# Optimization experiments

Hardware: AMD Instinct MI355X
Metric: run time of the kernel (lower is better)

## Reference

```python
import jax, jax.numpy as jnp
import numpy as np

LMAX = 10
F_IN = 64
F_OUT = 64
N_GRID = 512
IRREP_DIM = sum((2 * l + 1) ** 2 for l in range(LMAX + 1))  # 1771
BATCH = 256


def setup_inputs() -> dict:
    key = jax.random.key(0)
    kx, kD, kw = jax.random.split(key, 3)
    x = jax.random.normal(kx, (BATCH, F_IN, IRREP_DIM), dtype=jnp.float32)
    D = jax.random.normal(kD, (N_GRID, IRREP_DIM), dtype=jnp.float32)
    w = jax.random.normal(kw, (F_IN, F_OUT, N_GRID), dtype=jnp.float32)
    return {"x": x, "D": D, "w": w}


def _so3_linear(x, psi):
    # x:   (B, f_in, sum_l (2l+1)^2) signal over SO(3) irreps
    # psi: (f_in, f_out, sum_l (2l+1)^2) per-degree block weights
    B, f_in, _ = x.shape
    f_out = psi.shape[1]
    outs = []
    off = 0
    for l in range(LMAX + 1):
        d = 2 * l + 1
        blk = d * d
        # input block: multiplicity u (=d) x irrep component m (=d)
        x_l = x[:, :, off:off + blk].reshape(B, f_in, d, d)        # (B,i,u,m)
        w_l = psi[:, :, off:off + blk].reshape(f_in, f_out, d, d)  # (i,o,u,v)
        alpha = 1.0 / np.sqrt(f_in * d)  # e3nn fan-in path normalization
        out_l = jnp.einsum('bium,iouv->bovm', x_l, w_l) * alpha
        outs.append(out_l.reshape(B, f_out, blk))
        off += blk
    return jnp.concatenate(outs, axis=-1)


def reference(x, D, w):
    # project spatial filter into Fourier (irrep) domain
    n_grid = D.shape[0]
    psi = jnp.einsum('ni,xyn->xyi', D, w) / np.sqrt(n_grid)  # (f_in, f_out, IRREP_DIM)
    return _so3_linear(x, psi)
```

## Files before the change

kernel.cpp:

```cpp
#include <hip/hip_runtime.h>
#include <hip/hip_bf16.h>

#define IDIM 1771
#define NF 64
#define NG 512

constexpr int OFFS[12] = {0, 1, 10, 35, 84, 165, 286, 455, 680, 969, 1330, 1771};

typedef float f32x4 __attribute__((ext_vector_type(4)));
typedef float f32x2 __attribute__((ext_vector_type(2)));
typedef __bf16 bf16x2 __attribute__((ext_vector_type(2)));
typedef __bf16 bf16x8 __attribute__((ext_vector_type(8)));

__device__ __forceinline__ void gl_lds16(const void* g, void* l) {
    __builtin_amdgcn_global_load_lds((const __attribute__((address_space(1))) void*)g,
                                     (__attribute__((address_space(3))) void*)l, 16, 0, 0);
}

__global__ __launch_bounds__(256) void prep_repack_kernel(const float* __restrict__ D,
                                                          const float* __restrict__ w,
                                                          const float* __restrict__ x,
                                                          __bf16* __restrict__ Dt,
                                                          __bf16* __restrict__ wb,
                                                          __hip_bfloat16* __restrict__ A) {
    __shared__ alignas(16) char smem[16640];
    const int blk = blockIdx.x;
    const int t = threadIdx.x;
    const int lane = t & 63, grp = t >> 6;

    if (blk < 224) {
        float (*T)[65] = (float (*)[65])smem;
        const int ct = blk >> 3, nt = blk & 7;
        const int c0 = ct * 64, n0 = nt * 64;
        for (int nn = grp; nn < 64; nn += 4) {
            int c = c0 + lane;
            T[nn][lane] = (c < IDIM) ? D[(n0 + nn) * IDIM + c] : 0.0f;
        }
        __syncthreads();
        for (int cc = grp; cc < 64; cc += 4) {
            int c = c0 + cc;
            if (c < IDIM) Dt[c * NG + n0 + lane] = (__bf16)T[lane][cc];
        }
    } else if (blk < 288) {
        const int o = blk - 224;
#pragma unroll 4
        for (int ii = 0; ii < 64; ++ii) {
            f32x2 v = *(const f32x2*)&w[((size_t)(ii * 64 + o)) * NG + t * 2];
            bf16x2 ov;
            ov.x = (__bf16)v.x;
            ov.y = (__bf16)v.y;
            *(bf16x2*)&wb[((size_t)(o * 64 + ii)) * NG + t * 2] = ov;
        }
    } else {
        const int idx = blk - 288;
        const int l = idx >> 8;
        const int b = idx & 255;
        const int d = 2 * l + 1, off = OFFS[l], csq = d * d, Kp = 64 * d;
        __hip_bfloat16 (*T)[66] = (__hip_bfloat16 (*)[66])smem;
        const float* xb = x + (size_t)b * NF * IDIM + off;
        __hip_bfloat16* Ab = A + (size_t)16384 * off + (size_t)b * d * Kp;

        for (int c0 = 0; c0 < csq; c0 += 64) {
            for (int ii = grp; ii < 64; ii += 4) {
                int c = c0 + lane;
                float v = (c < csq) ? xb[ii * IDIM + c] : 0.0f;
                T[ii][lane] = __float2bfloat16(v);
            }
            __syncthreads();
            for (int cc = grp; cc < 64; cc += 4) {
                int c = c0 + cc;
                if (c < csq) {
                    int u = c / d, m = c - u * d;
                    Ab[(size_t)m * Kp + u * 64 + lane] = T[lane][cc];
                }
            }
            __syncthreads();
        }
    }
}

__global__ __launch_bounds__(256) void psi_mfma_kernel(const __bf16* __restrict__ Dt,
                                                       const __bf16* __restrict__ wb,
                                                       __bf16* __restrict__ Bm) {
    __shared__ alignas(16) __bf16 As[128 * 32];
    __shared__ alignas(16) __bf16 Bs[128 * 32];

    const int t = threadIdx.x, w = t >> 6, ln = t & 63;
    const int row0 = blockIdx.x * 128;
    const int col0 = blockIdx.y * 128;

    const __bf16* gp[4];
    __bf16* lp[4];
#pragma unroll
    for (int q = 0; q < 4; ++q) {
        int chunk = w * 4 + q;
        bool isA = chunk < 8;
        int j = isA ? chunk : chunk - 8;
        int r16 = j * 16 + (ln >> 2);
        int g = isA ? (row0 + r16 < IDIM ? row0 + r16 : IDIM - 1) : (col0 + r16);
        gp[q] = (isA ? Dt : wb) + (size_t)g * NG + (ln & 3) * 8;
        lp[q] = (isA ? As : Bs) + j * 512;
    }

    f32x4 acc[4][4];
    f32x4 zero = {0.0f, 0.0f, 0.0f, 0.0f};
#pragma unroll
    for (int i = 0; i < 4; ++i)
#pragma unroll
        for (int j = 0; j < 4; ++j) acc[i][j] = zero;

    const int wr = (w >> 1) * 64, wc = (w & 1) * 64;
    const int fr = ln & 15, kh = ln >> 4;

    for (int kt = 0; kt < NG; kt += 32) {
        __syncthreads();
#pragma unroll
        for (int q = 0; q < 4; ++q) {
            gl_lds16(gp[q], lp[q]);
            gp[q] += 32;
        }
        __syncthreads();

        bf16x8 af[4], bfr[4];
#pragma unroll
        for (int mt = 0; mt < 4; ++mt)
            af[mt] = *(const bf16x8*)&As[(wr + mt * 16 + fr) * 32 + kh * 8];
#pragma unroll
        for (int nt = 0; nt < 4; ++nt)
            bfr[nt] = *(const bf16x8*)&Bs[(wc + nt * 16 + fr) * 32 + kh * 8];
#pragma unroll
        for (int mt = 0; mt < 4; ++mt)
#pragma unroll
            for (int nt = 0; nt < 4; ++nt)
                acc[mt][nt] = __builtin_amdgcn_mfma_f32_16x16x32_bf16(af[mt], bfr[nt],
                                                                      acc[mt][nt], 0, 0, 0);
    }

    const float s = 0.04419417382415922f;
    const int o = (col0 + wc) >> 6;
#pragma unroll
    for (int mt = 0; mt < 4; ++mt) {
#pragma unroll
        for (int e = 0; e < 4; ++e) {
            int c = row0 + wr + mt * 16 + kh * 4 + e;
            if (c < IDIM) {
                int l = 0;
#pragma unroll
                for (int ll = 1; ll < 11; ++ll)
                    if (c >= OFFS[ll]) l = ll;
                int d = 2 * l + 1, off = OFFS[l];
                int rem = c - off;
                int u = (unsigned)rem / (unsigned)d;
                int v = rem - u * d;
                __bf16* bb = Bm + (size_t)4096 * off + (size_t)(o * d + v) * (64 * d) + u * 64;
#pragma unroll
                for (int nt = 0; nt < 4; ++nt) {
                    int i = nt * 16 + fr;
                    bb[i] = (__bf16)(acc[mt][nt][e] * s);
                }
            }
        }
    }
}

__global__ __launch_bounds__(256) void so3_gemm_all(const __bf16* __restrict__ A,
                                                    const __bf16* __restrict__ Bm,
                                                    float* __restrict__ out) {
    const int bid = blockIdx.x;
    const int v_ = (bid & 7) * 237 + (bid >> 3);
    if (v_ >= 1892) return;

    int l = 10, base = 0;
    if (v_ >= 462)  { l = 9; base = 462; }
    if (v_ >= 842)  { l = 8; base = 842; }
    if (v_ >= 1148) { l = 7; base = 1148; }
    if (v_ >= 1388) { l = 6; base = 1388; }
    if (v_ >= 1570) { l = 5; base = 1570; }
    if (v_ >= 1702) { l = 4; base = 1702; }
    if (v_ >= 1792) { l = 3; base = 1792; }
    if (v_ >= 1848) { l = 2; base = 1848; }
    if (v_ >= 1878) { l = 1; base = 1878; }
    if (v_ >= 1890) { l = 0; base = 1890; }

    const int d = 2 * l + 1;
    const int off = OFFS[l];
    const int Np = 64 * d, Kp = 64 * d;
    const int ntiles = l + 1;
    const int rel = v_ - base;
    const int bx = (unsigned)rel / (unsigned)ntiles;
    const int by = rel - bx * ntiles;
    const int row0 = bx * 128, col0 = by * 128;

    constexpr float ALPHA[11] = {0.125f, 0.07216878f, 0.05590170f, 0.04724556f,
                                 0.04166667f, 0.03768892f, 0.03466879f, 0.03227486f,
                                 0.03031695f, 0.02867697f, 0.02727724f};

    __shared__ alignas(16) __bf16 As[128 * 32];
    __shared__ alignas(16) __bf16 Bs[128 * 32];

    const int t = threadIdx.x, w = t >> 6, ln = t & 63;

    const __bf16* Abase = A + (size_t)16384 * off;
    const __bf16* Bbase = Bm + (size_t)4096 * off;

    const __bf16* gp[4];
    __bf16* lp[4];
#pragma unroll
    for (int q = 0; q < 4; ++q) {
        int chunk = w * 4 + q;
        bool isA = chunk < 8;
        int j = isA ? chunk : chunk - 8;
        int r16 = j * 16 + (ln >> 2);
        int g = isA ? (row0 + r16) : (col0 + r16 < Np ? col0 + r16 : Np - 1);
        gp[q] = (isA ? Abase : Bbase) + (size_t)g * Kp + (ln & 3) * 8;
        lp[q] = (isA ? As : Bs) + j * 512;
    }

    f32x4 acc[4][4];
    f32x4 zero = {0.0f, 0.0f, 0.0f, 0.0f};
#pragma unroll
    for (int i = 0; i < 4; ++i)
#pragma unroll
        for (int j = 0; j < 4; ++j) acc[i][j] = zero;

    const int wr = (w >> 1) * 64, wc = (w & 1) * 64;
    const int fr = ln & 15, kh = ln >> 4;

    for (int kt = 0; kt < Kp; kt += 32) {
        __syncthreads();
#pragma unroll
        for (int q = 0; q < 4; ++q) {
            gl_lds16(gp[q], lp[q]);
            gp[q] += 32;
        }
        __syncthreads();

        bf16x8 af[4], bfr[4];
#pragma unroll
        for (int mt = 0; mt < 4; ++mt)
            af[mt] = *(const bf16x8*)&As[(wr + mt * 16 + fr) * 32 + kh * 8];
#pragma unroll
        for (int nt = 0; nt < 4; ++nt)
            bfr[nt] = *(const bf16x8*)&Bs[(wc + nt * 16 + fr) * 32 + kh * 8];
#pragma unroll
        for (int mt = 0; mt < 4; ++mt)
#pragma unroll
            for (int nt = 0; nt < 4; ++nt)
                acc[mt][nt] = __builtin_amdgcn_mfma_f32_16x16x32_bf16(af[mt], bfr[nt],
                                                                      acc[mt][nt], 0, 0, 0);
    }

    __syncthreads();
    float* Tw = (float*)As + w * 256;
    const float alpha = ALPHA[l];

#pragma unroll
    for (int mt = 0; mt < 4; ++mt) {
        int r = row0 + wr + mt * 16 + fr;
        int b = (unsigned)r / (unsigned)d;
        int m = r - b * d;
        float* ob = out + (size_t)b * NF * IDIM + off + m;
#pragma unroll
        for (int nt = 0; nt < 4; ++nt) {
#pragma unroll
            for (int e = 0; e < 4; ++e) Tw[(kh * 4 + e) * 16 + fr] = acc[mt][nt][e];
            f32x4 vals = *(const f32x4*)&Tw[fr * 16 + kh * 4];
            int qb = col0 + wc + nt * 16 + kh * 4;
            int o = (unsigned)qb / (unsigned)d;
            int vv = qb - o * d;
#pragma unroll
            for (int j = 0; j < 4; ++j) {
                if (qb + j < Np) ob[o * IDIM + vv * d] = alpha * vals[j];
                ++vv;
                if (vv == d) { vv = 0; ++o; }
            }
        }
    }
}

extern "C" void kernel_launch(void* const* d_in, const int* in_sizes, int n_in,
                              void* d_out, int out_size, void* d_ws, size_t ws_size,
                              hipStream_t stream) {
    const float* x = (const float*)d_in[0];
    const float* D = (const float*)d_in[1];
    const float* w = (const float*)d_in[2];
    float* out = (float*)d_out;

    char* ws = (char*)d_ws;
    const size_t DT_BYTES = (size_t)IDIM * NG * 2;
    const size_t WB_BYTES = (size_t)4096 * NG * 2;
    const size_t A_BYTES = (size_t)16384 * IDIM * 2;

    __bf16* Dt = (__bf16*)ws;
    __bf16* wb = (__bf16*)(ws + DT_BYTES);
    __hip_bfloat16* A = (__hip_bfloat16*)(ws + DT_BYTES + WB_BYTES);
    __bf16* Bm = (__bf16*)(ws + DT_BYTES + WB_BYTES + A_BYTES);

    prep_repack_kernel<<<3104, 256, 0, stream>>>(D, w, x, Dt, wb, A);
    psi_mfma_kernel<<<dim3(14, 32), 256, 0, stream>>>(Dt, wb, Bm);
    so3_gemm_all<<<1896, 256, 0, stream>>>((const __bf16*)A, Bm, out);
}
```

Measured before the change: 413.5 us.

## Double-buffer LDS tiles in both MFMA GEMMs and vectorize the x repack stores

Both bf16 MFMA GEMM kernels switch from single-buffered shared tiles to a two-stage ping-pong buffer. The next K-slice is issued with global_load_lds before the MFMAs on the current slice run, and one waitcnt plus barrier per iteration replaces the two syncthreads. Separately, the x repack now builds 8-element bf16 vectors from the transposed tile and writes 16-byte stores instead of scalar 2-byte ones. The GEMM change doubles LDS per block, which may lower occupancy.

```diff
diff --git a/kernel.cpp b/kernel.cpp
--- a/kernel.cpp
+++ b/kernel.cpp
@@ -56,22 +56,29 @@
         const int l = idx >> 8;
         const int b = idx & 255;
         const int d = 2 * l + 1, off = OFFS[l], csq = d * d, Kp = 64 * d;
-        __hip_bfloat16 (*T)[66] = (__hip_bfloat16 (*)[66])smem;
+        __bf16 (*T)[66] = (__bf16 (*)[66])smem;
         const float* xb = x + (size_t)b * NF * IDIM + off;
-        __hip_bfloat16* Ab = A + (size_t)16384 * off + (size_t)b * d * Kp;
+        __bf16* Ab = (__bf16*)(A + (size_t)16384 * off + (size_t)b * d * Kp);
 
         for (int c0 = 0; c0 < csq; c0 += 64) {
             for (int ii = grp; ii < 64; ii += 4) {
                 int c = c0 + lane;
                 float v = (c < csq) ? xb[ii * IDIM + c] : 0.0f;
-                T[ii][lane] = __float2bfloat16(v);
+                T[ii][lane] = (__bf16)v;
             }
             __syncthreads();
-            for (int cc = grp; cc < 64; cc += 4) {
-                int c = c0 + cc;
+#pragma unroll
+            for (int s = 0; s < 2; ++s) {
+                int idx2 = s * 256 + t;
+                int c_loc = idx2 >> 3, i0 = (idx2 & 7) * 8;
+                int c = c0 + c_loc;
                 if (c < csq) {
-                    int u = c / d, m = c - u * d;
-                    Ab[(size_t)m * Kp + u * 64 + lane] = T[lane][cc];
+                    int u = (unsigned)c / (unsigned)d;
+                    int m = c - u * d;
+                    bf16x8 v;
+#pragma unroll
+                    for (int j = 0; j < 8; ++j) v[j] = T[i0 + j][c_loc];
+                    *(bf16x8*)(Ab + (size_t)m * Kp + u * 64 + i0) = v;
                 }
             }
             __syncthreads();
@@ -82,8 +89,7 @@
 __global__ __launch_bounds__(256) void psi_mfma_kernel(const __bf16* __restrict__ Dt,
                                                        const __bf16* __restrict__ wb,
                                                        __bf16* __restrict__ Bm) {
-    __shared__ alignas(16) __bf16 As[128 * 32];
-    __shared__ alignas(16) __bf16 Bs[128 * 32];
+    __shared__ alignas(16) __bf16 S[4][4096];
 
     const int t = threadIdx.x, w = t >> 6, ln = t & 63;
     const int row0 = blockIdx.x * 128;
@@ -95,11 +101,11 @@
     for (int q = 0; q < 4; ++q) {
         int chunk = w * 4 + q;
         bool isA = chunk < 8;
-        int j = isA ? chunk : chunk - 8;
+        int j = chunk & 7;
         int r16 = j * 16 + (ln >> 2);
         int g = isA ? (row0 + r16 < IDIM ? row0 + r16 : IDIM - 1) : (col0 + r16);
         gp[q] = (isA ? Dt : wb) + (size_t)g * NG + (ln & 3) * 8;
-        lp[q] = (isA ? As : Bs) + j * 512;
+        lp[q] = S[isA ? 0 : 1] + j * 512;
     }
 
     f32x4 acc[4][4];
@@ -112,28 +118,40 @@
     const int wr = (w >> 1) * 64, wc = (w & 1) * 64;
     const int fr = ln & 15, kh = ln >> 4;
 
+#pragma unroll
+    for (int q = 0; q < 4; ++q) { gl_lds16(gp[q], lp[q]); gp[q] += 32; }
+    asm volatile("s_waitcnt vmcnt(0)" ::: "memory");
+    __builtin_amdgcn_s_barrier();
+    __builtin_amdgcn_sched_barrier(0);
+
+    int cur = 0;
     for (int kt = 0; kt < NG; kt += 32) {
-        __syncthreads();
-#pragma unroll
-        for (int q = 0; q < 4; ++q) {
-            gl_lds16(gp[q], lp[q]);
-            gp[q] += 32;
-        }
-        __syncthreads();
-
+        if (kt + 32 < NG) {
+#pragma unroll
+            for (int q = 0; q < 4; ++q) {
+                gl_lds16(gp[q], lp[q] + (cur ^ 1) * 8192);
+                gp[q] += 32;
+            }
+        }
+        const __bf16* As_ = S[cur * 2];
+        const __bf16* Bs_ = S[cur * 2 + 1];
         bf16x8 af[4], bfr[4];
 #pragma unroll
         for (int mt = 0; mt < 4; ++mt)
-            af[mt] = *(const bf16x8*)&As[(wr + mt * 16 + fr) * 32 + kh * 8];
+            af[mt] = *(const bf16x8*)&As_[(wr + mt * 16 + fr) * 32 + kh * 8];
 #pragma unroll
         for (int nt = 0; nt < 4; ++nt)
-            bfr[nt] = *(const bf16x8*)&Bs[(wc + nt * 16 + fr) * 32 + kh * 8];
+            bfr[nt] = *(const bf16x8*)&Bs_[(wc + nt * 16 + fr) * 32 + kh * 8];
 #pragma unroll
         for (int mt = 0; mt < 4; ++mt)
 #pragma unroll
             for (int nt = 0; nt < 4; ++nt)
                 acc[mt][nt] = __builtin_amdgcn_mfma_f32_16x16x32_bf16(af[mt], bfr[nt],
                                                                       acc[mt][nt], 0, 0, 0);
+        asm volatile("s_waitcnt vmcnt(0)" ::: "memory");
+        __builtin_amdgcn_s_barrier();
+        __builtin_amdgcn_sched_barrier(0);
+        cur ^= 1;
     }
 
     const float s = 0.04419417382415922f;
@@ -195,8 +213,7 @@
                                  0.04166667f, 0.03768892f, 0.03466879f, 0.03227486f,
                                  0.03031695f, 0.02867697f, 0.02727724f};
 
-    __shared__ alignas(16) __bf16 As[128 * 32];
-    __shared__ alignas(16) __bf16 Bs[128 * 32];
+    __shared__ alignas(16) __bf16 S[4][4096];
 
     const int t = threadIdx.x, w = t >> 6, ln = t & 63;
 
@@ -209,11 +226,11 @@
     for (int q = 0; q < 4; ++q) {
         int chunk = w * 4 + q;
         bool isA = chunk < 8;
-        int j = isA ? chunk : chunk - 8;
+        int j = chunk & 7;
         int r16 = j * 16 + (ln >> 2);
         int g = isA ? (row0 + r16) : (col0 + r16 < Np ? col0 + r16 : Np - 1);
         gp[q] = (isA ? Abase : Bbase) + (size_t)g * Kp + (ln & 3) * 8;
-        lp[q] = (isA ? As : Bs) + j * 512;
+        lp[q] = S[isA ? 0 : 1] + j * 512;
     }
 
     f32x4 acc[4][4];
@@ -226,32 +243,44 @@
     const int wr = (w >> 1) * 64, wc = (w & 1) * 64;
     const int fr = ln & 15, kh = ln >> 4;
 
+#pragma unroll
+    for (int q = 0; q < 4; ++q) { gl_lds16(gp[q], lp[q]); gp[q] += 32; }
+    asm volatile("s_waitcnt vmcnt(0)" ::: "memory");
+    __builtin_amdgcn_s_barrier();
+    __builtin_amdgcn_sched_barrier(0);
+
+    int cur = 0;
     for (int kt = 0; kt < Kp; kt += 32) {
-        __syncthreads();
-#pragma unroll
-        for (int q = 0; q < 4; ++q) {
-            gl_lds16(gp[q], lp[q]);
-            gp[q] += 32;
-        }
-        __syncthreads();
-
+        if (kt + 32 < Kp) {
+#pragma unroll
+            for (int q = 0; q < 4; ++q) {
+                gl_lds16(gp[q], lp[q] + (cur ^ 1) * 8192);
+                gp[q] += 32;
+            }
+        }
+        const __bf16* As_ = S[cur * 2];
+        const __bf16* Bs_ = S[cur * 2 + 1];
         bf16x8 af[4], bfr[4];
 #pragma unroll
         for (int mt = 0; mt < 4; ++mt)
-            af[mt] = *(const bf16x8*)&As[(wr + mt * 16 + fr) * 32 + kh * 8];
+            af[mt] = *(const bf16x8*)&As_[(wr + mt * 16 + fr) * 32 + kh * 8];
 #pragma unroll
         for (int nt = 0; nt < 4; ++nt)
-            bfr[nt] = *(const bf16x8*)&Bs[(wc + nt * 16 + fr) * 32 + kh * 8];
+            bfr[nt] = *(const bf16x8*)&Bs_[(wc + nt * 16 + fr) * 32 + kh * 8];
 #pragma unroll
         for (int mt = 0; mt < 4; ++mt)
 #pragma unroll
             for (int nt = 0; nt < 4; ++nt)
                 acc[mt][nt] = __builtin_amdgcn_mfma_f32_16x16x32_bf16(af[mt], bfr[nt],
                                                                       acc[mt][nt], 0, 0, 0);
+        asm volatile("s_waitcnt vmcnt(0)" ::: "memory");
+        __builtin_amdgcn_s_barrier();
+        __builtin_amdgcn_sched_barrier(0);
+        cur ^= 1;
     }
 
     __syncthreads();
-    float* Tw = (float*)As + w * 256;
+    float* Tw = (float*)S + w * 256;
     const float alpha = ALPHA[l];
 
 #pragma unroll
```

After: 395.4 us. 4.4% less time.
